# Performance work log

Hardware: AMD Instinct MI355X
Metric: run time of the kernel (lower is better)

The kernel has to match this reference:

```python
import jax, jax.numpy as jnp
import numpy as np

T = 2
TEMPERATURE = 1.0


def _softor(x, axis):
    # probabilistic soft-OR: 1 - prod(1 - x), clamped to [0, 1]
    return jnp.clip(1.0 - jnp.prod(1.0 - x, axis=axis), 0.0, 1.0)


def setup_inputs() -> dict:
    key = jax.random.key(0)
    k1, k2, k3, k4 = jax.random.split(key, 4)
    B, C, G, BODY, M = 32, 128, 4096, 4, 5
    v0 = jax.random.uniform(k1, (B, G), dtype=jnp.float32)
    X = jax.random.randint(k2, (C, G, BODY), 0, G, dtype=jnp.int64)
    fact_mask = jax.random.randint(k3, (C, G), 0, 2).astype(bool)
    W = jax.random.normal(k4, (M, C), dtype=jnp.float32)
    return {"v0": v0, "X": X, "fact_mask": fact_mask, "W": W}


def reference(v0, X, fact_mask, W):
    # W_mat[m, c] = softmax over clauses per program slot
    W_mat = jax.nn.softmax(W / TEMPERATURE, axis=-1)
    v = v0  # [B, G]
    for _ in range(T):
        gathered = v[:, X]                      # [B, C, G, body] gather
        clause_vals = jnp.prod(gathered, -1)    # [B, C, G] product over body
        clause_vals = jnp.where(fact_mask[None], 1.0, clause_vals)
        h = jnp.einsum('mc,bcg->bmg', W_mat, clause_vals)  # [B, M, G]
        r = _softor(h, axis=1)                  # [B, G]
        v = _softor(jnp.stack([v, r], axis=1), axis=1)
    return v
```

## Files before the change

kernel.cpp:

```cpp
#include <hip/hip_runtime.h>
#include <math.h>

#define B_TOT 32
#define C_TOT 128
#define G_TOT 4096
#define BODY  4
#define M_TOT 5

#define B_PER 4
#define CQ    8
#define GPB   64
#define THREADS (GPB*CQ)
#define C_PER (C_TOT/CQ)

__global__ void softmax_w_kernel(const float* __restrict__ W, float* __restrict__ Wm) {
    const int lane = threadIdx.x;
    for (int m = 0; m < M_TOT; ++m) {
        float a = W[m * C_TOT + lane];
        float b = W[m * C_TOT + lane + 64];
        float mx = fmaxf(a, b);
        #pragma unroll
        for (int off = 32; off; off >>= 1) mx = fmaxf(mx, __shfl_xor(mx, off));
        float ea = expf(a - mx), eb = expf(b - mx);
        float s = ea + eb;
        #pragma unroll
        for (int off = 32; off; off >>= 1) s += __shfl_xor(s, off);
        Wm[m * C_TOT + lane]      = ea / s;
        Wm[m * C_TOT + lane + 64] = eb / s;
    }
}

__global__ __launch_bounds__(THREADS, 4) void step_kernel(
    const float* __restrict__ v_in,
    const int*   __restrict__ X,
    const int*   __restrict__ fact,
    const float* __restrict__ Wm,
    float*       __restrict__ v_out)
{
    __shared__ float lv[B_PER][G_TOT];
    __shared__ float lw[M_TOT][C_TOT];

    const int tid = threadIdx.x;
    const int b0  = blockIdx.y * B_PER;
    const int gt  = blockIdx.x * GPB;

    for (int i = tid; i < M_TOT * C_TOT; i += THREADS)
        ((float*)lw)[i] = Wm[i];
    {
        const float4* vsrc = (const float4*)(v_in + (size_t)b0 * G_TOT);
        float4* vdst = (float4*)&lv[0][0];
        #pragma unroll
        for (int i = tid; i < B_PER * G_TOT / 4; i += THREADS)
            vdst[i] = vsrc[i];
    }
    __syncthreads();

    const int cq = tid & (CQ - 1);
    const int gl = tid >> 3;
    const int g  = gt + gl;

    float h[M_TOT][B_PER];
    #pragma unroll
    for (int m = 0; m < M_TOT; ++m)
        #pragma unroll
        for (int b = 0; b < B_PER; ++b) h[m][b] = 0.0f;

    const int cbase = cq * C_PER;
    #pragma unroll 4
    for (int ci = 0; ci < C_PER; ++ci) {
        const int c = cbase + ci;
        const int4 xi = ((const int4*)X)[(size_t)c * G_TOT + g];
        const int  fm = fact[(size_t)c * G_TOT + g];
        const float w0 = lw[0][c], w1 = lw[1][c], w2 = lw[2][c],
                    w3 = lw[3][c], w4 = lw[4][c];
        #pragma unroll
        for (int b = 0; b < B_PER; ++b) {
            float p = lv[b][xi.x] * lv[b][xi.y] * lv[b][xi.z] * lv[b][xi.w];
            p = fm ? 1.0f : p;
            h[0][b] += w0 * p;
            h[1][b] += w1 * p;
            h[2][b] += w2 * p;
            h[3][b] += w3 * p;
            h[4][b] += w4 * p;
        }
    }

    #pragma unroll
    for (int m = 0; m < M_TOT; ++m)
        #pragma unroll
        for (int b = 0; b < B_PER; ++b) {
            float s = h[m][b];
            s += __shfl_xor(s, 1);
            s += __shfl_xor(s, 2);
            s += __shfl_xor(s, 4);
            h[m][b] = s;
        }

    if (cq == 0) {
        #pragma unroll
        for (int b = 0; b < B_PER; ++b) {
            float om = 1.0f;
            #pragma unroll
            for (int m = 0; m < M_TOT; ++m) om *= (1.0f - h[m][b]);
            float r = 1.0f - om;
            r = fminf(fmaxf(r, 0.0f), 1.0f);
            const float vold = lv[b][g];
            float vn = 1.0f - (1.0f - vold) * (1.0f - r);
            vn = fminf(fmaxf(vn, 0.0f), 1.0f);
            v_out[(size_t)(b0 + b) * G_TOT + g] = vn;
        }
    }
}

extern "C" void kernel_launch(void* const* d_in, const int* in_sizes, int n_in,
                              void* d_out, int out_size, void* d_ws, size_t ws_size,
                              hipStream_t stream) {
    const float* v0   = (const float*)d_in[0];
    const int*   X    = (const int*)  d_in[1];
    const int*   fact = (const int*)  d_in[2];
    const float* W    = (const float*)d_in[3];
    float*       out  = (float*)d_out;

    float* wm = (float*)d_ws;
    float* v1 = (float*)d_ws + 1024;

    softmax_w_kernel<<<1, 64, 0, stream>>>(W, wm);

    dim3 grid(G_TOT / GPB, B_TOT / B_PER);
    step_kernel<<<grid, THREADS, 0, stream>>>(v0, X, fact, wm, v1);
    step_kernel<<<grid, THREADS, 0, stream>>>(v1, X, fact, wm, out);
}
```

Measured before the change: 49.08 us.

## Interleave batch values in LDS as float4 and use packed FP32 math

The shared-memory copy of v becomes a [G][4] interleaved float4 layout, so each gathered index fetches all four batch values in one 128-bit LDS read instead of four scalar reads. Softmax weights are stored transposed ([C][8]) so each clause's five weights are contiguous. Products and accumulations use v_pk_mul_f32/v_pk_fma_f32 through inline asm. Clause assignment is interleaved across the 8 lanes (c = ci*CQ+cq), and the final epilogue is spread over four lanes, one per batch, instead of one lane doing all four. The staging loop now does strided scalar global loads to transpose v, and LDS usage for weights grows slightly.

```diff
diff --git a/kernel.cpp b/kernel.cpp
--- a/kernel.cpp
+++ b/kernel.cpp
@@ -13,7 +13,18 @@
 #define THREADS (GPB*CQ)
 #define C_PER (C_TOT/CQ)
 
-__global__ void softmax_w_kernel(const float* __restrict__ W, float* __restrict__ Wm) {
+typedef float f32x2 __attribute__((ext_vector_type(2)));
+
+__device__ __forceinline__ f32x2 pk_mul(f32x2 a, f32x2 b) {
+    f32x2 d;
+    asm("v_pk_mul_f32 %0, %1, %2" : "=v"(d) : "v"(a), "v"(b));
+    return d;
+}
+__device__ __forceinline__ void pk_fma(f32x2& d, f32x2 a, f32x2 b) {
+    asm("v_pk_fma_f32 %0, %1, %2, %0" : "+v"(d) : "v"(a), "v"(b));
+}
+
+__global__ void softmax_w_kernel(const float* __restrict__ W, float* __restrict__ Wt) {
     const int lane = threadIdx.x;
     for (int m = 0; m < M_TOT; ++m) {
         float a = W[m * C_TOT + lane];
@@ -25,8 +36,8 @@
         float s = ea + eb;
         #pragma unroll
         for (int off = 32; off; off >>= 1) s += __shfl_xor(s, off);
-        Wm[m * C_TOT + lane]      = ea / s;
-        Wm[m * C_TOT + lane + 64] = eb / s;
+        Wt[lane * 8 + m]        = ea / s;
+        Wt[(lane + 64) * 8 + m] = eb / s;
     }
 }
 
@@ -34,24 +45,25 @@
     const float* __restrict__ v_in,
     const int*   __restrict__ X,
     const int*   __restrict__ fact,
-    const float* __restrict__ Wm,
+    const float* __restrict__ Wt,
     float*       __restrict__ v_out)
 {
-    __shared__ float lv[B_PER][G_TOT];
-    __shared__ float lw[M_TOT][C_TOT];
+    __shared__ float4 lv4[G_TOT];
+    __shared__ float  lwt[C_TOT * 8];
 
     const int tid = threadIdx.x;
     const int b0  = blockIdx.y * B_PER;
     const int gt  = blockIdx.x * GPB;
 
-    for (int i = tid; i < M_TOT * C_TOT; i += THREADS)
-        ((float*)lw)[i] = Wm[i];
-    {
-        const float4* vsrc = (const float4*)(v_in + (size_t)b0 * G_TOT);
-        float4* vdst = (float4*)&lv[0][0];
-        #pragma unroll
-        for (int i = tid; i < B_PER * G_TOT / 4; i += THREADS)
-            vdst[i] = vsrc[i];
+    for (int i = tid; i < C_TOT * 8; i += THREADS) lwt[i] = Wt[i];
+
+    for (int g = tid; g < G_TOT; g += THREADS) {
+        float4 t;
+        t.x = v_in[(size_t)(b0 + 0) * G_TOT + g];
+        t.y = v_in[(size_t)(b0 + 1) * G_TOT + g];
+        t.z = v_in[(size_t)(b0 + 2) * G_TOT + g];
+        t.w = v_in[(size_t)(b0 + 3) * G_TOT + g];
+        lv4[g] = t;
     }
     __syncthreads();
 
@@ -59,56 +71,68 @@
     const int gl = tid >> 3;
     const int g  = gt + gl;
 
-    float h[M_TOT][B_PER];
+    f32x2 hlo[M_TOT], hhi[M_TOT];
     #pragma unroll
-    for (int m = 0; m < M_TOT; ++m)
-        #pragma unroll
-        for (int b = 0; b < B_PER; ++b) h[m][b] = 0.0f;
+    for (int m = 0; m < M_TOT; ++m) { hlo[m] = (f32x2){0.f, 0.f}; hhi[m] = (f32x2){0.f, 0.f}; }
 
-    const int cbase = cq * C_PER;
+    const f32x2 one2 = (f32x2){1.f, 1.f};
+
     #pragma unroll 4
     for (int ci = 0; ci < C_PER; ++ci) {
-        const int c = cbase + ci;
+        const int c = ci * CQ + cq;
         const int4 xi = ((const int4*)X)[(size_t)c * G_TOT + g];
         const int  fm = fact[(size_t)c * G_TOT + g];
-        const float w0 = lw[0][c], w1 = lw[1][c], w2 = lw[2][c],
-                    w3 = lw[3][c], w4 = lw[4][c];
+        const float* wp = &lwt[c * 8];
+
+        const float4 va = lv4[xi.x];
+        const float4 vb = lv4[xi.y];
+        const float4 vc = lv4[xi.z];
+        const float4 vd = lv4[xi.w];
+
+        f32x2 plo = pk_mul(pk_mul((f32x2){va.x, va.y}, (f32x2){vb.x, vb.y}),
+                           pk_mul((f32x2){vc.x, vc.y}, (f32x2){vd.x, vd.y}));
+        f32x2 phi = pk_mul(pk_mul((f32x2){va.z, va.w}, (f32x2){vb.z, vb.w}),
+                           pk_mul((f32x2){vc.z, vc.w}, (f32x2){vd.z, vd.w}));
+        plo = fm ? one2 : plo;
+        phi = fm ? one2 : phi;
+
         #pragma unroll
-        for (int b = 0; b < B_PER; ++b) {
-            float p = lv[b][xi.x] * lv[b][xi.y] * lv[b][xi.z] * lv[b][xi.w];
-            p = fm ? 1.0f : p;
-            h[0][b] += w0 * p;
-            h[1][b] += w1 * p;
-            h[2][b] += w2 * p;
-            h[3][b] += w3 * p;
-            h[4][b] += w4 * p;
+        for (int m = 0; m < M_TOT; ++m) {
+            const float w = wp[m];
+            const f32x2 ws = (f32x2){w, w};
+            pk_fma(hlo[m], plo, ws);
+            pk_fma(hhi[m], phi, ws);
         }
     }
 
+    float hs[M_TOT][B_PER];
+    #pragma unroll
+    for (int m = 0; m < M_TOT; ++m) {
+        hs[m][0] = hlo[m].x; hs[m][1] = hlo[m].y;
+        hs[m][2] = hhi[m].x; hs[m][3] = hhi[m].y;
+    }
     #pragma unroll
     for (int m = 0; m < M_TOT; ++m)
         #pragma unroll
         for (int b = 0; b < B_PER; ++b) {
-            float s = h[m][b];
+            float s = hs[m][b];
             s += __shfl_xor(s, 1);
             s += __shfl_xor(s, 2);
             s += __shfl_xor(s, 4);
-            h[m][b] = s;
+            hs[m][b] = s;
         }
 
-    if (cq == 0) {
+    if (cq < B_PER) {
+        const int b = cq;
+        float om = 1.0f;
         #pragma unroll
-        for (int b = 0; b < B_PER; ++b) {
-            float om = 1.0f;
-            #pragma unroll
-            for (int m = 0; m < M_TOT; ++m) om *= (1.0f - h[m][b]);
-            float r = 1.0f - om;
-            r = fminf(fmaxf(r, 0.0f), 1.0f);
-            const float vold = lv[b][g];
-            float vn = 1.0f - (1.0f - vold) * (1.0f - r);
-            vn = fminf(fmaxf(vn, 0.0f), 1.0f);
-            v_out[(size_t)(b0 + b) * G_TOT + g] = vn;
-        }
+        for (int m = 0; m < M_TOT; ++m) om *= (1.0f - hs[m][b]);
+        float r = 1.0f - om;
+        r = fminf(fmaxf(r, 0.0f), 1.0f);
+        const float vold = ((const float*)lv4)[g * 4 + b];
+        float vn = 1.0f - (1.0f - vold) * (1.0f - r);
+        vn = fminf(fmaxf(vn, 0.0f), 1.0f);
+        v_out[(size_t)(b0 + b) * G_TOT + g] = vn;
     }
 }
 
@@ -121,12 +145,12 @@
     const float* W    = (const float*)d_in[3];
     float*       out  = (float*)d_out;
 
-    float* wm = (float*)d_ws;
+    float* wt = (float*)d_ws;
     float* v1 = (float*)d_ws + 1024;
 
-    softmax_w_kernel<<<1, 64, 0, stream>>>(W, wm);
+    softmax_w_kernel<<<1, 64, 0, stream>>>(W, wt);
 
     dim3 grid(G_TOT / GPB, B_TOT / B_PER);
-    step_kernel<<<grid, THREADS, 0, stream>>>(v0, X, fact, wm, v1);
-    step_kernel<<<grid, THREADS, 0, stream>>>(v1, X, fact, wm, out);
+    step_kernel<<<grid, THREADS, 0, stream>>>(v0, X, fact, wt, v1);
+    step_kernel<<<grid, THREADS, 0, stream>>>(v1, X, fact, wt, out);
 }
```

New measurement: 43.98 us. 10.4% less time.
